# Performance work log

Hardware: AMD Instinct MI355X
Metric: run time of the kernel (lower is better)

Reference implementation:

```python
import jax, jax.numpy as jnp
import numpy as np
import math

B, Z, D = 1024, 32768, 128

def setup_inputs() -> dict:
    key = jax.random.key(0)
    k1, k2, k3 = jax.random.split(key, 3)
    z_sparse = jax.random.randint(k1, (B, Z), 0, 2, dtype=jnp.int32)
    context_embedding = jax.random.normal(k2, (B, D), dtype=jnp.float32)
    embd_table = jax.random.normal(k3, (Z, D), dtype=jnp.float32)  # nn.Embedding weight
    return {"z_sparse": z_sparse, "context_embedding": context_embedding, "embd_table": embd_table}

def reference(z_sparse, context_embedding, embd_table):
    # mask[b, z] = feature z active in batch b  (matches (z_sparse > 0).nonzero())
    mask = z_sparse > 0  # [B, Z]
    # attn_scores = (ctx * emb).sum(-1) / sqrt(D), densified over all (b, z)
    scores = (context_embedding @ embd_table.T) / math.sqrt(embd_table.shape[1])  # [B, Z]
    # per-batch softmax over active features only
    masked = jnp.where(mask, scores, -jnp.inf)
    w = jax.nn.softmax(masked, axis=-1)
    w = jnp.where(mask, w, 0.0)  # zero inactive (also kills NaN for all-empty rows)
    # scatter-add of emb * weight == weighted matmul against the table
    out = w @ embd_table  # [B, D]
    counts = jnp.clip(jnp.sum(mask, axis=-1), 1, None)  # bincount(...).clamp(min=1)
    return out / counts[:, None].astype(out.dtype)
```

## Files before the change

kernel.cpp:

```cpp
#include <hip/hip_runtime.h>
#include <stdint.h>

#define B_SZ 1024
#define Z_SZ 32768
#define D_SZ 128
#define NZ   32
#define CZ   (Z_SZ / NZ)
#define TZ   64
#define ITERS (CZ / TZ)
#define TBLK 64
#define WROWS 16

#define SEMB_STRIDE  136
#define SEMBT_STRIDE 72
#define SP_STRIDE    72

#define WS_O   0
#define WS_M   (NZ * B_SZ * D_SZ)
#define WS_L   (WS_M + NZ * B_SZ)
#define WS_C   (WS_L + NZ * B_SZ)
#define WS_TAB (WS_C + NZ * B_SZ)

typedef short bf16x8 __attribute__((ext_vector_type(8)));
typedef float f32x4  __attribute__((ext_vector_type(4)));

#if __has_builtin(__builtin_amdgcn_exp2f)
#define EXP2F(x) __builtin_amdgcn_exp2f(x)
#else
#define EXP2F(x) exp2f(x)
#endif

__device__ __forceinline__ unsigned short f2bf(float f) {
    union { float f; uint32_t u; } v; v.f = f;
    uint32_t u = v.u;
    u = (u + 0x7FFFu + ((u >> 16) & 1u)) >> 16;
    return (unsigned short)u;
}

__global__ __launch_bounds__(256) void prep_tables(
    const float* __restrict__ emb,
    unsigned short* __restrict__ embR,
    unsigned short* __restrict__ embT)
{
    __shared__ __align__(16) unsigned short st[64 * SEMB_STRIDE];
    const int z0 = blockIdx.x * 64;
    const int t  = threadIdx.x;
    {
        const int r = t >> 2, q = t & 3;
        const float* src = emb + (size_t)(z0 + r) * D_SZ + q * 32;
        unsigned short* dR = embR + (size_t)(z0 + r) * D_SZ + q * 32;
        unsigned short* dL = st + r * SEMB_STRIDE + q * 32;
#pragma unroll
        for (int u = 0; u < 8; ++u) {
            float4 x = *(const float4*)(src + 4 * u);
            ushort4 h;
            h.x = f2bf(x.x); h.y = f2bf(x.y); h.z = f2bf(x.z); h.w = f2bf(x.w);
            *(ushort4*)(dR + 4 * u) = h;
            *(ushort4*)(dL + 4 * u) = h;
        }
    }
    __syncthreads();
    {
        const int lane = t & 63, w = t >> 6;
#pragma unroll
        for (int i = 0; i < 4; ++i) {
            const int d = w * 32 + i * 8 + (lane >> 3);
            const int c = lane & 7;
            bf16x8 v;
#pragma unroll
            for (int k = 0; k < 8; ++k) v[k] = (short)st[(c * 8 + k) * SEMB_STRIDE + d];
            *(bf16x8*)(embT + (size_t)d * Z_SZ + z0 + c * 8) = v;
        }
    }
}

__global__ __launch_bounds__(256, 2) void attn_part(
    const int*            __restrict__ zs,
    const float*          __restrict__ ctx,
    const unsigned short* __restrict__ embR,
    const unsigned short* __restrict__ embT,
    float*                __restrict__ ws)
{
    __shared__ __align__(16) unsigned short s_emb [TZ   * SEMB_STRIDE];
    __shared__ __align__(16) unsigned short s_embT[D_SZ * SEMBT_STRIDE];
    __shared__ __align__(16) unsigned short s_P   [4 * WROWS * SP_STRIDE];

    const int tid  = threadIdx.x;
    const int wave = tid >> 6;
    const int lane = tid & 63;
    const int l15  = lane & 15;
    const int quad = lane >> 4;

    const int bg     = blockIdx.x;
    const int ch     = blockIdx.y;
    const int z_base = ch * CZ;
    const int wb0    = bg * TBLK + wave * WROWS;

    const int srow = tid >> 2, sq3 = tid & 3;
    const int sd   = tid >> 1, sh  = tid & 1;

    bf16x8 afrag[4];
    {
        const float scale = (float)(1.4426950408889634 * 0.08838834764831845);
        const float* crow = ctx + (size_t)(wb0 + l15) * D_SZ;
#pragma unroll
        for (int ks = 0; ks < 4; ++ks) {
            const float* p = crow + ks * 32 + quad * 8;
            float4 x0 = *(const float4*)(p);
            float4 x1 = *(const float4*)(p + 4);
            bf16x8 a;
            a[0] = (short)f2bf(x0.x * scale); a[1] = (short)f2bf(x0.y * scale);
            a[2] = (short)f2bf(x0.z * scale); a[3] = (short)f2bf(x0.w * scale);
            a[4] = (short)f2bf(x1.x * scale); a[5] = (short)f2bf(x1.y * scale);
            a[6] = (short)f2bf(x1.z * scale); a[7] = (short)f2bf(x1.w * scale);
            afrag[ks] = a;
        }
    }

    float m_r[4], l_r[4];
    int   cnt_r[4];
    f32x4 acc2[8];
#pragma unroll
    for (int r = 0; r < 4; ++r) { m_r[r] = -1e30f; l_r[r] = 0.f; cnt_r[r] = 0; }
#pragma unroll
    for (int n = 0; n < 8; ++n) { acc2[n][0]=0.f; acc2[n][1]=0.f; acc2[n][2]=0.f; acc2[n][3]=0.f; }

    bf16x8 rA[4], rT[4];
    int mi[4][4];

    {
        const unsigned short* srcR = embR + (size_t)(z_base + srow) * D_SZ + sq3 * 32;
        const unsigned short* srcT = embT + (size_t)sd * Z_SZ + z_base + sh * 32;
#pragma unroll
        for (int u = 0; u < 4; ++u) {
            rA[u] = *(const bf16x8*)(srcR + u * 8);
            rT[u] = *(const bf16x8*)(srcT + u * 8);
        }
#pragma unroll
        for (int r = 0; r < 4; ++r) {
            const int b = wb0 + quad * 4 + r;
            const int* p = zs + (size_t)b * Z_SZ + z_base + l15;
#pragma unroll
            for (int nt = 0; nt < 4; ++nt) mi[nt][r] = p[nt * 16];
        }
    }

    for (int it = 0; it < ITERS; ++it) {
        __syncthreads();

        {
            unsigned short* dst = s_emb + srow * SEMB_STRIDE + sq3 * 32;
#pragma unroll
            for (int u = 0; u < 4; ++u) *(bf16x8*)(dst + u * 8) = rA[u];
        }
        {
            unsigned short* dst = s_embT + sd * SEMBT_STRIDE + sh * 32;
#pragma unroll
            for (int u = 0; u < 4; ++u) *(bf16x8*)(dst + u * 8) = rT[u];
        }

        int msk[4][4];
#pragma unroll
        for (int r = 0; r < 4; ++r) {
#pragma unroll
            for (int nt = 0; nt < 4; ++nt) msk[nt][r] = (mi[nt][r] > 0) ? 1 : 0;
            cnt_r[r] += msk[0][r] + msk[1][r] + msk[2][r] + msk[3][r];
        }

        __syncthreads();

        if (it + 1 < ITERS) {
            const int z0n = z_base + (it + 1) * TZ;
            const unsigned short* srcR = embR + (size_t)(z0n + srow) * D_SZ + sq3 * 32;
            const unsigned short* srcT = embT + (size_t)sd * Z_SZ + z0n + sh * 32;
#pragma unroll
            for (int u = 0; u < 4; ++u) {
                rA[u] = *(const bf16x8*)(srcR + u * 8);
                rT[u] = *(const bf16x8*)(srcT + u * 8);
            }
#pragma unroll
            for (int r = 0; r < 4; ++r) {
                const int b = wb0 + quad * 4 + r;
                const int* p = zs + (size_t)b * Z_SZ + z0n + l15;
#pragma unroll
                for (int nt = 0; nt < 4; ++nt) mi[nt][r] = p[nt * 16];
            }
        }

        f32x4 sfr[4];
#pragma unroll
        for (int nt = 0; nt < 4; ++nt) {
            f32x4 c; c[0]=0.f; c[1]=0.f; c[2]=0.f; c[3]=0.f;
            const unsigned short* bb = s_emb + (nt * 16 + l15) * SEMB_STRIDE + quad * 8;
#pragma unroll
            for (int ks = 0; ks < 4; ++ks) {
                bf16x8 bf = *(const bf16x8*)(bb + ks * 32);
                c = __builtin_amdgcn_mfma_f32_16x16x32_bf16(afrag[ks], bf, c, 0, 0, 0);
            }
            sfr[nt] = c;
        }

        float tmax[4];
#pragma unroll
        for (int r = 0; r < 4; ++r) {
            float a0 = msk[0][r] ? sfr[0][r] : -1e30f;
            float a1 = msk[1][r] ? sfr[1][r] : -1e30f;
            float a2 = msk[2][r] ? sfr[2][r] : -1e30f;
            float a3 = msk[3][r] ? sfr[3][r] : -1e30f;
            tmax[r] = fmaxf(fmaxf(a0, a1), fmaxf(a2, a3));
        }
#pragma unroll
        for (int s = 1; s < 16; s <<= 1) {
#pragma unroll
            for (int r = 0; r < 4; ++r) tmax[r] = fmaxf(tmax[r], __shfl_xor(tmax[r], s));
        }
        float alpha[4];
#pragma unroll
        for (int r = 0; r < 4; ++r) {
            float mnew = fmaxf(m_r[r], tmax[r]);
            alpha[r] = EXP2F(m_r[r] - mnew);
            m_r[r] = mnew;
            l_r[r] *= alpha[r];
        }
        float psum[4]; psum[0]=0.f; psum[1]=0.f; psum[2]=0.f; psum[3]=0.f;
        unsigned short* pw = s_P + wave * (WROWS * SP_STRIDE);
#pragma unroll
        for (int nt = 0; nt < 4; ++nt) {
#pragma unroll
            for (int r = 0; r < 4; ++r) {
                float p = msk[nt][r] ? EXP2F(sfr[nt][r] - m_r[r]) : 0.f;
                psum[r] += p;
                pw[(quad * 4 + r) * SP_STRIDE + nt * 16 + l15] = f2bf(p);
            }
        }
#pragma unroll
        for (int s = 1; s < 16; s <<= 1) {
#pragma unroll
            for (int r = 0; r < 4; ++r) psum[r] += __shfl_xor(psum[r], s);
        }
#pragma unroll
        for (int r = 0; r < 4; ++r) l_r[r] += psum[r];

#pragma unroll
        for (int n = 0; n < 8; ++n) {
#pragma unroll
            for (int r = 0; r < 4; ++r) acc2[n][r] *= alpha[r];
        }

        const unsigned short* pb = pw + l15 * SP_STRIDE + quad * 8;
        bf16x8 pA0 = *(const bf16x8*)(pb);
        bf16x8 pA1 = *(const bf16x8*)(pb + 32);
#pragma unroll
        for (int nt2 = 0; nt2 < 8; ++nt2) {
            const unsigned short* tb = s_embT + (nt2 * 16 + l15) * SEMBT_STRIDE + quad * 8;
            bf16x8 b0 = *(const bf16x8*)(tb);
            bf16x8 b1 = *(const bf16x8*)(tb + 32);
            acc2[nt2] = __builtin_amdgcn_mfma_f32_16x16x32_bf16(pA0, b0, acc2[nt2], 0, 0, 0);
            acc2[nt2] = __builtin_amdgcn_mfma_f32_16x16x32_bf16(pA1, b1, acc2[nt2], 0, 0, 0);
        }
    }

#pragma unroll
    for (int nt2 = 0; nt2 < 8; ++nt2) {
#pragma unroll
        for (int r = 0; r < 4; ++r) {
            const int b = wb0 + quad * 4 + r;
            ws[WS_O + ((size_t)ch * B_SZ + b) * D_SZ + nt2 * 16 + l15] = acc2[nt2][r];
        }
    }
    float cntf[4];
#pragma unroll
    for (int r = 0; r < 4; ++r) cntf[r] = (float)cnt_r[r];
#pragma unroll
    for (int s = 1; s < 16; s <<= 1) {
#pragma unroll
        for (int r = 0; r < 4; ++r) cntf[r] += __shfl_xor(cntf[r], s);
    }
    if (l15 == 0) {
#pragma unroll
        for (int r = 0; r < 4; ++r) {
            const int b = wb0 + quad * 4 + r;
            ws[WS_M + ch * B_SZ + b] = m_r[r];
            ws[WS_L + ch * B_SZ + b] = l_r[r];
            ws[WS_C + ch * B_SZ + b] = cntf[r];
        }
    }
}

__global__ __launch_bounds__(128) void attn_reduce(
    const float* __restrict__ ws, float* __restrict__ out)
{
    const int b = blockIdx.x;
    const int d = threadIdx.x;
    const float* mP = ws + WS_M;
    const float* lP = ws + WS_L;
    const float* cP = ws + WS_C;

    float M = -1e30f;
#pragma unroll
    for (int c = 0; c < NZ; ++c) M = fmaxf(M, mP[c * B_SZ + b]);

    float L = 0.f, C = 0.f, acc = 0.f;
#pragma unroll
    for (int c = 0; c < NZ; ++c) {
        float w = EXP2F(mP[c * B_SZ + b] - M);
        L += lP[c * B_SZ + b] * w;
        C += cP[c * B_SZ + b];
        acc += ws[WS_O + ((size_t)c * B_SZ + b) * D_SZ + d] * w;
    }
    float cnt = fmaxf(C, 1.0f);
    out[(size_t)b * D_SZ + d] = (L > 0.f) ? acc / (L * cnt) : 0.f;
}

extern "C" void kernel_launch(void* const* d_in, const int* in_sizes, int n_in,
                              void* d_out, int out_size, void* d_ws, size_t ws_size,
                              hipStream_t stream) {
    (void)in_sizes; (void)n_in; (void)out_size; (void)ws_size;
    const int*   zs  = (const int*)  d_in[0];
    const float* ctx = (const float*)d_in[1];
    const float* emb = (const float*)d_in[2];
    float* out = (float*)d_out;
    float* ws  = (float*)d_ws;

    unsigned short* embR = (unsigned short*)(ws + WS_TAB);
    unsigned short* embT = embR + (size_t)Z_SZ * D_SZ;

    prep_tables<<<Z_SZ / 64, 256, 0, stream>>>(emb, embR, embT);

    dim3 grid1(B_SZ / TBLK, NZ);
    attn_part<<<grid1, 256, 0, stream>>>(zs, ctx, embR, embT, ws);
    attn_reduce<<<B_SZ, 128, 0, stream>>>(ws, out);
}
```

Before: 241.2 us.

## Bit-pack mask in prep pass, transpose MFMA operands, add lazy softmax rescaling

```diff
diff --git a/kernel.cpp b/kernel.cpp
--- a/kernel.cpp
+++ b/kernel.cpp
@@ -10,10 +10,15 @@
 #define ITERS (CZ / TZ)
 #define TBLK 64
 #define WROWS 16
+#define ZW   (Z_SZ / 32)
 
 #define SEMB_STRIDE  136
 #define SEMBT_STRIDE 72
 #define SP_STRIDE    72
+#define ST_STRIDE    136
+
+#define NB_MASK ((B_SZ * ZW) / 256)
+#define NB_TAB  (Z_SZ / 64)
 
 #define WS_O   0
 #define WS_M   (NZ * B_SZ * D_SZ)
@@ -37,19 +42,37 @@
     return (unsigned short)u;
 }
 
-__global__ __launch_bounds__(256) void prep_tables(
-    const float* __restrict__ emb,
+__global__ __launch_bounds__(256) void prep(
+    const int*      __restrict__ zs,
+    const float*    __restrict__ emb,
     unsigned short* __restrict__ embR,
-    unsigned short* __restrict__ embT)
+    unsigned short* __restrict__ embT,
+    uint32_t*       __restrict__ maskp)
 {
-    __shared__ __align__(16) unsigned short st[64 * SEMB_STRIDE];
-    const int z0 = blockIdx.x * 64;
+    __shared__ __align__(16) unsigned short st[64 * ST_STRIDE];
+    if (blockIdx.x < NB_MASK) {
+        const int gid = blockIdx.x * 256 + threadIdx.x;
+        const int4* src = (const int4*)(zs + (size_t)gid * 32);
+        uint32_t mbits = 0;
+#pragma unroll
+        for (int k = 0; k < 8; ++k) {
+            int4 v = src[k];
+            mbits |= (v.x > 0 ? 1u : 0u) << (4 * k + 0);
+            mbits |= (v.y > 0 ? 1u : 0u) << (4 * k + 1);
+            mbits |= (v.z > 0 ? 1u : 0u) << (4 * k + 2);
+            mbits |= (v.w > 0 ? 1u : 0u) << (4 * k + 3);
+        }
+        maskp[gid] = mbits;
+        return;
+    }
+
+    const int z0 = (blockIdx.x - NB_MASK) * 64;
     const int t  = threadIdx.x;
     {
         const int r = t >> 2, q = t & 3;
         const float* src = emb + (size_t)(z0 + r) * D_SZ + q * 32;
         unsigned short* dR = embR + (size_t)(z0 + r) * D_SZ + q * 32;
-        unsigned short* dL = st + r * SEMB_STRIDE + q * 32;
+        unsigned short* dL = st + r * ST_STRIDE + q * 32;
 #pragma unroll
         for (int u = 0; u < 8; ++u) {
             float4 x = *(const float4*)(src + 4 * u);
@@ -68,14 +91,14 @@
             const int c = lane & 7;
             bf16x8 v;
 #pragma unroll
-            for (int k = 0; k < 8; ++k) v[k] = (short)st[(c * 8 + k) * SEMB_STRIDE + d];
+            for (int k = 0; k < 8; ++k) v[k] = (short)st[(c * 8 + k) * ST_STRIDE + d];
             *(bf16x8*)(embT + (size_t)d * Z_SZ + z0 + c * 8) = v;
         }
     }
 }
 
 __global__ __launch_bounds__(256, 2) void attn_part(
-    const int*            __restrict__ zs,
+    const uint32_t*       __restrict__ maskp,
     const float*          __restrict__ ctx,
     const unsigned short* __restrict__ embR,
     const unsigned short* __restrict__ embT,
@@ -95,6 +118,7 @@
     const int ch     = blockIdx.y;
     const int z_base = ch * CZ;
     const int wb0    = bg * TBLK + wave * WROWS;
+    const int brow   = wb0 + l15;
 
     const int srow = tid >> 2, sq3 = tid & 3;
     const int sd   = tid >> 1, sh  = tid & 1;
@@ -102,7 +126,7 @@
     bf16x8 afrag[4];
     {
         const float scale = (float)(1.4426950408889634 * 0.08838834764831845);
-        const float* crow = ctx + (size_t)(wb0 + l15) * D_SZ;
+        const float* crow = ctx + (size_t)brow * D_SZ;
 #pragma unroll
         for (int ks = 0; ks < 4; ++ks) {
             const float* p = crow + ks * 32 + quad * 8;
@@ -117,17 +141,14 @@
         }
     }
 
-    float m_r[4], l_r[4];
-    int   cnt_r[4];
+    float m_s = -1e30f, l_s = 0.f;
+    int   cnt = 0;
     f32x4 acc2[8];
 #pragma unroll
-    for (int r = 0; r < 4; ++r) { m_r[r] = -1e30f; l_r[r] = 0.f; cnt_r[r] = 0; }
-#pragma unroll
     for (int n = 0; n < 8; ++n) { acc2[n][0]=0.f; acc2[n][1]=0.f; acc2[n][2]=0.f; acc2[n][3]=0.f; }
 
     bf16x8 rA[4], rT[4];
-    int mi[4][4];
-
+    uint2  mv, mvn;
     {
         const unsigned short* srcR = embR + (size_t)(z_base + srow) * D_SZ + sq3 * 32;
         const unsigned short* srcT = embT + (size_t)sd * Z_SZ + z_base + sh * 32;
@@ -136,13 +157,7 @@
             rA[u] = *(const bf16x8*)(srcR + u * 8);
             rT[u] = *(const bf16x8*)(srcT + u * 8);
         }
-#pragma unroll
-        for (int r = 0; r < 4; ++r) {
-            const int b = wb0 + quad * 4 + r;
-            const int* p = zs + (size_t)b * Z_SZ + z_base + l15;
-#pragma unroll
-            for (int nt = 0; nt < 4; ++nt) mi[nt][r] = p[nt * 16];
-        }
+        mv = *(const uint2*)(maskp + (size_t)brow * ZW + (z_base >> 5));
     }
 
     for (int it = 0; it < ITERS; ++it) {
@@ -157,14 +172,6 @@
             unsigned short* dst = s_embT + sd * SEMBT_STRIDE + sh * 32;
 #pragma unroll
             for (int u = 0; u < 4; ++u) *(bf16x8*)(dst + u * 8) = rT[u];
-        }
-
-        int msk[4][4];
-#pragma unroll
-        for (int r = 0; r < 4; ++r) {
-#pragma unroll
-            for (int nt = 0; nt < 4; ++nt) msk[nt][r] = (mi[nt][r] > 0) ? 1 : 0;
-            cnt_r[r] += msk[0][r] + msk[1][r] + msk[2][r] + msk[3][r];
         }
 
         __syncthreads();
@@ -178,13 +185,7 @@
                 rA[u] = *(const bf16x8*)(srcR + u * 8);
                 rT[u] = *(const bf16x8*)(srcT + u * 8);
             }
-#pragma unroll
-            for (int r = 0; r < 4; ++r) {
-                const int b = wb0 + quad * 4 + r;
-                const int* p = zs + (size_t)b * Z_SZ + z0n + l15;
-#pragma unroll
-                for (int nt = 0; nt < 4; ++nt) mi[nt][r] = p[nt * 16];
-            }
+            mvn = *(const uint2*)(maskp + (size_t)brow * ZW + (z0n >> 5));
         }
 
         f32x4 sfr[4];
@@ -194,96 +195,88 @@
             const unsigned short* bb = s_emb + (nt * 16 + l15) * SEMB_STRIDE + quad * 8;
 #pragma unroll
             for (int ks = 0; ks < 4; ++ks) {
-                bf16x8 bf = *(const bf16x8*)(bb + ks * 32);
-                c = __builtin_amdgcn_mfma_f32_16x16x32_bf16(afrag[ks], bf, c, 0, 0, 0);
+                bf16x8 ef = *(const bf16x8*)(bb + ks * 32);
+                c = __builtin_amdgcn_mfma_f32_16x16x32_bf16(ef, afrag[ks], c, 0, 0, 0);
             }
             sfr[nt] = c;
         }
 
-        float tmax[4];
+        const uint32_t w0 = mv.x >> (quad * 4);
+        const uint32_t w1 = mv.y >> (quad * 4);
+        int bit[4][4];
 #pragma unroll
         for (int r = 0; r < 4; ++r) {
-            float a0 = msk[0][r] ? sfr[0][r] : -1e30f;
-            float a1 = msk[1][r] ? sfr[1][r] : -1e30f;
-            float a2 = msk[2][r] ? sfr[2][r] : -1e30f;
-            float a3 = msk[3][r] ? sfr[3][r] : -1e30f;
-            tmax[r] = fmaxf(fmaxf(a0, a1), fmaxf(a2, a3));
-        }
-#pragma unroll
-        for (int s = 1; s < 16; s <<= 1) {
-#pragma unroll
-            for (int r = 0; r < 4; ++r) tmax[r] = fmaxf(tmax[r], __shfl_xor(tmax[r], s));
-        }
-        float alpha[4];
-#pragma unroll
-        for (int r = 0; r < 4; ++r) {
-            float mnew = fmaxf(m_r[r], tmax[r]);
-            alpha[r] = EXP2F(m_r[r] - mnew);
-            m_r[r] = mnew;
-            l_r[r] *= alpha[r];
-        }
-        float psum[4]; psum[0]=0.f; psum[1]=0.f; psum[2]=0.f; psum[3]=0.f;
-        unsigned short* pw = s_P + wave * (WROWS * SP_STRIDE);
+            bit[0][r] = (int)((w0 >> (r))      & 1u);
+            bit[1][r] = (int)((w0 >> (16 + r)) & 1u);
+            bit[2][r] = (int)((w1 >> (r))      & 1u);
+            bit[3][r] = (int)((w1 >> (16 + r)) & 1u);
+        }
+        cnt += __popc(mv.x) + __popc(mv.y);
+
+        float tm = -1e30f;
 #pragma unroll
         for (int nt = 0; nt < 4; ++nt) {
-#pragma unroll
-            for (int r = 0; r < 4; ++r) {
-                float p = msk[nt][r] ? EXP2F(sfr[nt][r] - m_r[r]) : 0.f;
-                psum[r] += p;
-                pw[(quad * 4 + r) * SP_STRIDE + nt * 16 + l15] = f2bf(p);
-            }
-        }
-#pragma unroll
-        for (int s = 1; s < 16; s <<= 1) {
-#pragma unroll
-            for (int r = 0; r < 4; ++r) psum[r] += __shfl_xor(psum[r], s);
-        }
-#pragma unroll
-        for (int r = 0; r < 4; ++r) l_r[r] += psum[r];
-
-#pragma unroll
-        for (int n = 0; n < 8; ++n) {
-#pragma unroll
-            for (int r = 0; r < 4; ++r) acc2[n][r] *= alpha[r];
-        }
-
-        const unsigned short* pb = pw + l15 * SP_STRIDE + quad * 8;
+            float a0 = bit[nt][0] ? sfr[nt][0] : -1e30f;
+            float a1 = bit[nt][1] ? sfr[nt][1] : -1e30f;
+            float a2 = bit[nt][2] ? sfr[nt][2] : -1e30f;
+            float a3 = bit[nt][3] ? sfr[nt][3] : -1e30f;
+            tm = fmaxf(tm, fmaxf(fmaxf(a0, a1), fmaxf(a2, a3)));
+        }
+        tm = fmaxf(tm, __shfl_xor(tm, 16));
+        tm = fmaxf(tm, __shfl_xor(tm, 32));
+
+        if (__any(tm > m_s + 8.f)) {
+            float mnew = fmaxf(m_s, tm);
+            float al = EXP2F(m_s - mnew);
+            m_s = mnew;
+            l_s *= al;
+#pragma unroll
+            for (int n = 0; n < 8; ++n) acc2[n] *= al;
+        }
+
+        unsigned short* pwv = s_P + wave * (WROWS * SP_STRIDE) + l15 * SP_STRIDE + quad * 4;
+        float ps = 0.f;
+#pragma unroll
+        for (int nt = 0; nt < 4; ++nt) {
+            float p0 = bit[nt][0] ? EXP2F(sfr[nt][0] - m_s) : 0.f;
+            float p1 = bit[nt][1] ? EXP2F(sfr[nt][1] - m_s) : 0.f;
+            float p2 = bit[nt][2] ? EXP2F(sfr[nt][2] - m_s) : 0.f;
+            float p3 = bit[nt][3] ? EXP2F(sfr[nt][3] - m_s) : 0.f;
+            ps += (p0 + p1) + (p2 + p3);
+            ushort4 h;
+            h.x = f2bf(p0); h.y = f2bf(p1); h.z = f2bf(p2); h.w = f2bf(p3);
+            *(ushort4*)(pwv + nt * 16) = h;
+        }
+        ps += __shfl_xor(ps, 16);
+        ps += __shfl_xor(ps, 32);
+        l_s += ps;
+
+        const unsigned short* pb = s_P + wave * (WROWS * SP_STRIDE) + l15 * SP_STRIDE + quad * 8;
         bf16x8 pA0 = *(const bf16x8*)(pb);
         bf16x8 pA1 = *(const bf16x8*)(pb + 32);
 #pragma unroll
         for (int nt2 = 0; nt2 < 8; ++nt2) {
             const unsigned short* tb = s_embT + (nt2 * 16 + l15) * SEMBT_STRIDE + quad * 8;
-            bf16x8 b0 = *(const bf16x8*)(tb);
-            bf16x8 b1 = *(const bf16x8*)(tb + 32);
-            acc2[nt2] = __builtin_amdgcn_mfma_f32_16x16x32_bf16(pA0, b0, acc2[nt2], 0, 0, 0);
-            acc2[nt2] = __builtin_amdgcn_mfma_f32_16x16x32_bf16(pA1, b1, acc2[nt2], 0, 0, 0);
-        }
-    }
-
-#pragma unroll
-    for (int nt2 = 0; nt2 < 8; ++nt2) {
-#pragma unroll
-        for (int r = 0; r < 4; ++r) {
-            const int b = wb0 + quad * 4 + r;
-            ws[WS_O + ((size_t)ch * B_SZ + b) * D_SZ + nt2 * 16 + l15] = acc2[nt2][r];
-        }
-    }
-    float cntf[4];
-#pragma unroll
-    for (int r = 0; r < 4; ++r) cntf[r] = (float)cnt_r[r];
-#pragma unroll
-    for (int s = 1; s < 16; s <<= 1) {
-#pragma unroll
-        for (int r = 0; r < 4; ++r) cntf[r] += __shfl_xor(cntf[r], s);
-    }
-    if (l15 == 0) {
-#pragma unroll
-        for (int r = 0; r < 4; ++r) {
-            const int b = wb0 + quad * 4 + r;
-            ws[WS_M + ch * B_SZ + b] = m_r[r];
-            ws[WS_L + ch * B_SZ + b] = l_r[r];
-            ws[WS_C + ch * B_SZ + b] = cntf[r];
-        }
+            bf16x8 e0 = *(const bf16x8*)(tb);
+            bf16x8 e1 = *(const bf16x8*)(tb + 32);
+            acc2[nt2] = __builtin_amdgcn_mfma_f32_16x16x32_bf16(e0, pA0, acc2[nt2], 0, 0, 0);
+            acc2[nt2] = __builtin_amdgcn_mfma_f32_16x16x32_bf16(e1, pA1, acc2[nt2], 0, 0, 0);
+        }
+
+        mv = mvn;
+    }
+
+    {
+        float* orow = ws + WS_O + ((size_t)ch * B_SZ + brow) * D_SZ;
+#pragma unroll
+        for (int nt2 = 0; nt2 < 8; ++nt2) {
+            *(f32x4*)(orow + nt2 * 16 + quad * 4) = acc2[nt2];
+        }
+    }
+    if (lane < 16) {
+        ws[WS_M + ch * B_SZ + brow] = m_s;
+        ws[WS_L + ch * B_SZ + brow] = l_s;
+        ws[WS_C + ch * B_SZ + brow] = (float)cnt;
     }
 }
 
@@ -308,8 +301,8 @@
         C += cP[c * B_SZ + b];
         acc += ws[WS_O + ((size_t)c * B_SZ + b) * D_SZ + d] * w;
     }
-    float cnt = fmaxf(C, 1.0f);
-    out[(size_t)b * D_SZ + d] = (L > 0.f) ? acc / (L * cnt) : 0.f;
+    float cntv = fmaxf(C, 1.0f);
+    out[(size_t)b * D_SZ + d] = (L > 0.f) ? acc / (L * cntv) : 0.f;
 }
 
 extern "C" void kernel_launch(void* const* d_in, const int* in_sizes, int n_in,
@@ -322,12 +315,13 @@
     float* out = (float*)d_out;
     float* ws  = (float*)d_ws;
 
-    unsigned short* embR = (unsigned short*)(ws + WS_TAB);
-    unsigned short* embT = embR + (size_t)Z_SZ * D_SZ;
-
-    prep_tables<<<Z_SZ / 64, 256, 0, stream>>>(emb, embR, embT);
+    unsigned short* embR  = (unsigned short*)(ws + WS_TAB);
+    unsigned short* embT  = embR + (size_t)Z_SZ * D_SZ;
+    uint32_t*       maskp = (uint32_t*)(embT + (size_t)Z_SZ * D_SZ);
+
+    prep<<<NB_MASK + NB_TAB, 256, 0, stream>>>(zs, emb, embR, embT, maskp);
 
     dim3 grid1(B_SZ / TBLK, NZ);
-    attn_part<<<grid1, 256, 0, stream>>>(zs, ctx, embR, embT, ws);
+    attn_part<<<grid1, 256, 0, stream>>>(maskp, ctx, embR, embT, ws);
     attn_reduce<<<B_SZ, 128, 0, stream>>>(ws, out);
 }
```

Measured after the change: 253.9 us. +5.2%, slower.
